# Optimization experiments

Hardware: AMD Instinct MI355X
Metric: run time of the kernel (lower is better)

The kernel has to match this reference:

```python
import jax, jax.numpy as jnp
import numpy as np


def _shift_kernel(dtype=jnp.float32):
    # IdealDelayKernels: 9 output channels, 8 one-hot 3x3 shift taps (center skipped), 9th all-zero
    k = np.zeros((9, 1, 1, 3, 3), np.float32)
    idx = -1
    for i in range(3):
        for j in range(3):
            if i == 1 and j == 1:
                continue
            idx += 1
            k[idx, 0, 0, i, j] = 1.0
    return jnp.asarray(k, dtype)


def _conv2d(x, w, b, pad):
    y = jax.lax.conv_general_dilated(x, w, (1, 1), [(pad, pad), (pad, pad)],
                                     dimension_numbers=('NCHW', 'OIHW', 'NCHW'))
    return y if b is None else y + b[None, :, None, None]


def setup_inputs() -> dict:
    key = jax.random.key(0)
    ks = jax.random.split(key, 16)
    B, C, H, W = 2, 19, 512, 512
    s = 0.1  # xavier-ish scale for small convs
    return {
        'x': jax.random.normal(ks[0], (B, C, H, W), jnp.float32),
        'image': jax.random.normal(ks[1], (B, 3, H, W), jnp.float32),
        # IntraNetwork(3 -> 16 -> 16 -> 19): conv3x3, conv3x3, conv1x1 (BN frozen at identity)
        'intra_w1': jax.random.normal(ks[2], (16, 3, 3, 3), jnp.float32) * s,
        'intra_b1': jnp.zeros((16,), jnp.float32),
        'intra_w2': jax.random.normal(ks[3], (16, 16, 3, 3), jnp.float32) * s,
        'intra_b2': jnp.zeros((16,), jnp.float32),
        'intra_w3': jax.random.normal(ks[4], (19, 16, 1, 1), jnp.float32) * s,
        'intra_b3': jnp.zeros((19,), jnp.float32),
        # GuidingNetwork(20 -> 32 -> 32 -> 11): conv3x3, conv3x3, conv1x1 + sigmoid
        'guide_w1': jax.random.normal(ks[5], (32, 20, 3, 3), jnp.float32) * s,
        'guide_b1': jnp.zeros((32,), jnp.float32),
        'guide_w2': jax.random.normal(ks[6], (32, 32, 3, 3), jnp.float32) * s,
        'guide_b2': jnp.zeros((32,), jnp.float32),
        'guide_w3': jax.random.normal(ks[7], (11, 32, 1, 1), jnp.float32) * s,
        'guide_b3': jnp.zeros((11,), jnp.float32),
    }


def reference(x, image, intra_w1, intra_b1, intra_w2, intra_b2, intra_w3, intra_b3,
              guide_w1, guide_b1, guide_w2, guide_b2, guide_w3, guide_b3):
    # intra_net: image -> [B,19,H,W] (frozen BN == identity)
    f = jax.nn.relu(_conv2d(image, intra_w1, intra_b1, 1))
    f = jax.nn.relu(_conv2d(f, intra_w2, intra_b2, 1))
    intra = _conv2d(f, intra_w3, intra_b3, 0)            # [B,19,H,W]

    # Laplacian edge on the argmax label map
    single_x = jnp.argmax(x, axis=1, keepdims=True).astype(x.dtype)  # [B,1,H,W]
    lapla = jnp.full((1, 1, 3, 3), 1.0, x.dtype).at[0, 0, 1, 1].set(-8.0)
    edge = _conv2d(single_x, lapla, None, 1)             # [B,1,H,W]

    # guiding network: cat(intra, edge) -> 11 per-pixel guide weights
    gi = jnp.concatenate([intra, edge], axis=1)          # [B,20,H,W]
    g = jax.nn.relu(_conv2d(gi, guide_w1, guide_b1, 1))
    g = jax.nn.relu(_conv2d(g, guide_w2, guide_b2, 1))
    g = jax.nn.sigmoid(_conv2d(g, guide_w3, guide_b3, 0))  # [B,11,H,W]
    guide_feat = g[:, :, None]                           # [B,11,1,H,W]
    guide_feat = guide_feat / (jnp.sum(guide_feat, axis=1, keepdims=True) + 1e-9)

    # shift-kernel conv3d: [B,1,19,H,W] -> [B,9,19,H,W]
    xs = x[:, None]
    short = jax.lax.conv_general_dilated(xs, _shift_kernel(x.dtype), (1, 1, 1),
                                         [(0, 0), (1, 1), (1, 1)],
                                         dimension_numbers=('NCDHW', 'OIDHW', 'NCDHW'))
    xcat = jnp.concatenate([xs, short, intra[:, None]], axis=1)  # [B,11,19,H,W]

    out = jnp.sum(guide_feat * xcat, axis=1)             # [B,19,H,W]
    return (out, guide_feat, edge)
```

## Files before the change

kernel.cpp:

```cpp
#include <hip/hip_runtime.h>
#include <math.h>

constexpr int H = 512, W = 512, B = 2;
constexpr int HW = H * W;

typedef __attribute__((ext_vector_type(8))) short short8;
typedef __attribute__((ext_vector_type(4))) float floatx4;
typedef __attribute__((ext_vector_type(4))) unsigned int uint4v;

__device__ inline unsigned short f2bf(float f) {
  union { float f; unsigned int u; } x{f};
  const unsigned int u = x.u;
  return (unsigned short)((u + 0x7FFFu + ((u >> 16) & 1u)) >> 16);
}
__device__ inline float bf2f(unsigned short s) {
  union { unsigned int u; float f; } x;
  x.u = (unsigned int)s << 16;
  return x.f;
}
__device__ inline void unpk2(unsigned int u, float& lo, float& hi) {
  union { unsigned int u; float f; } a, b;
  a.u = u << 16;
  b.u = u & 0xffff0000u;
  lo = a.f;
  hi = b.f;
}

template <int CIN, int COUT, bool RELU>
__global__ __launch_bounds__(256) void conv3x3_fp32_pack(
    const float* __restrict__ in0, const float* __restrict__ wgt,
    const float* __restrict__ bias, unsigned short* __restrict__ outp) {
  constexpr int TS = 16, TH = 18, LDW = 20;
  __shared__ float tile[CIN][TH][LDW];
  const int tx = threadIdx.x, ty = threadIdx.y;
  const int tid = ty * 16 + tx;
  const int w0 = blockIdx.x * TS, h0 = blockIdx.y * TS, b = blockIdx.z;

  for (int idx = tid; idx < CIN * TH * TH; idx += 256) {
    const int cin = idx / (TH * TH);
    const int rem = idx - cin * (TH * TH);
    const int r = rem / TH, c = rem - r * TH;
    const int gh = h0 + r - 1, gw = w0 + c - 1;
    float v = 0.f;
    if ((unsigned)gh < (unsigned)H && (unsigned)gw < (unsigned)W)
      v = in0[(size_t)(b * CIN + cin) * HW + gh * W + gw];
    tile[cin][r][c] = v;
  }
  __syncthreads();

  float acc[COUT];
#pragma unroll
  for (int co = 0; co < COUT; ++co) acc[co] = bias[co];
  for (int cin = 0; cin < CIN; ++cin) {
#pragma unroll
    for (int t = 0; t < 9; ++t) {
      const int ky = t / 3, kx = t - ky * 3;
      const float v = tile[cin][ty + ky][tx + kx];
#pragma unroll
      for (int co = 0; co < COUT; ++co)
        acc[co] = fmaf(v, wgt[(co * CIN + cin) * 9 + t], acc[co]);
    }
  }
  const int oh = h0 + ty, ow = w0 + tx;
  unsigned int pk[COUT / 2];
#pragma unroll
  for (int c2 = 0; c2 < COUT / 2; ++c2) {
    float a0 = acc[2 * c2], a1 = acc[2 * c2 + 1];
    if (RELU) { a0 = fmaxf(a0, 0.f); a1 = fmaxf(a1, 0.f); }
    pk[c2] = (unsigned)f2bf(a0) | ((unsigned)f2bf(a1) << 16);
  }
  unsigned short* dst = outp + ((size_t)(b * H + oh) * W + ow) * COUT;
#pragma unroll
  for (int u = 0; u < COUT / 8; ++u)
    *(uint4v*)(dst + u * 8) = uint4v{pk[u * 4], pk[u * 4 + 1], pk[u * 4 + 2], pk[u * 4 + 3]};
}

template <int CIN, int CINP, int COUT, int KS>
__global__ __launch_bounds__(256) void repack_w(
    const float* __restrict__ w, unsigned short* __restrict__ bp) {
  constexpr int NT = COUT / 16;
  const int idx = blockIdx.x * 256 + threadIdx.x;
  if (idx >= NT * KS * 512) return;
  const int j = idx & 7;
  const int l = (idx >> 3) & 63;
  const int ks = (idx >> 9) % KS;
  const int nt = idx / (KS * 512);
  const int co = nt * 16 + (l & 15);
  const int kglob = ks * 32 + (l >> 4) * 8 + j;
  const int tap = kglob / CINP;
  const int cin = kglob % CINP;
  float v = 0.f;
  if (tap < 9 && cin < CIN) v = w[((size_t)co * CIN + cin) * 9 + tap];
  bp[idx] = f2bf(v);
}

template <int CINP, int KS, int NT, bool EDGE19, int EPI>
__global__ __launch_bounds__(256) void conv3x3_mfma(
    const unsigned short* __restrict__ inp, const float* __restrict__ edg,
    const unsigned short* __restrict__ bpack, const float* __restrict__ bias,
    const float* __restrict__ ew, const float* __restrict__ eb,
    unsigned short* __restrict__ outp, float* __restrict__ outf) {
  constexpr int COUT = NT * 16;
  constexpr int CS = (CINP == 16) ? 24 : 40;
  constexpr int EPS = (EPI == 1) ? 24 : 40;
  constexpr int TR = 10;
  __shared__ __align__(16) unsigned short tile[TR * 34 * CS];

  const int tid = threadIdx.x;
  const int w0 = blockIdx.x * 32, h0 = blockIdx.y * 8, b = blockIdx.z;

  for (int idx = tid; idx < TR * 34; idx += 256) {
    const int r = idx / 34, c = idx - r * 34;
    const int gh = h0 + r - 1, gw = w0 + c - 1;
    unsigned short* dst = tile + (size_t)(r * 34 + c) * CS;
    if ((unsigned)gh < (unsigned)H && (unsigned)gw < (unsigned)W) {
      const unsigned short* src = inp + ((size_t)(b * H + gh) * W + gw) * CINP;
#pragma unroll
      for (int u = 0; u < CINP / 8; ++u)
        *(uint4v*)(dst + u * 8) = *(const uint4v*)(src + u * 8);
      if (EDGE19) dst[19] = f2bf(edg[(size_t)b * HW + gh * W + gw]);
    } else {
#pragma unroll
      for (int u = 0; u < CINP / 8; ++u)
        *(uint4v*)(dst + u * 8) = uint4v{0, 0, 0, 0};
    }
  }
  __syncthreads();

  const int wv = tid >> 6, lane = tid & 63;
  const int q = lane >> 4, l15 = lane & 15;
  const int rb = wv * 2;

  floatx4 acc[4][NT];
#pragma unroll
  for (int mf = 0; mf < 4; ++mf)
#pragma unroll
    for (int nt = 0; nt < NT; ++nt) acc[mf][nt] = floatx4{0.f, 0.f, 0.f, 0.f};

#pragma unroll
  for (int ks = 0; ks < KS; ++ks) {
    short8 bfrag[NT];
#pragma unroll
    for (int nt = 0; nt < NT; ++nt)
      bfrag[nt] = *(const short8*)(bpack + (size_t)(((nt * KS) + ks) * 64 + lane) * 8);

    const int kbase = ks * 32;
    const int kq = kbase + q * 8;
    int tapq = kq / CINP;
    const int cinq = kq % CINP;
    if (tapq > 8) tapq = 8;
    const int ky = tapq / 3, kx = tapq - ky * 3;
    const unsigned short* aptr =
        tile + (size_t)((rb + ky) * 34 + (l15 + kx)) * CS + cinq;

#pragma unroll
    for (int mf = 0; mf < 4; ++mf) {
      constexpr int mfs[4][2] = {{0, 0}, {0, 16}, {1, 0}, {1, 16}};
      const int off = (mfs[mf][0] * 34 + mfs[mf][1]) * CS;
      const short8 af = *(const short8*)(aptr + off);
#pragma unroll
      for (int nt = 0; nt < NT; ++nt)
        acc[mf][nt] = __builtin_amdgcn_mfma_f32_16x16x32_bf16(
            af, bfrag[nt], acc[mf][nt], 0, 0, 0);
    }
  }

  if constexpr (EPI == 0) {
#pragma unroll
    for (int nt = 0; nt < NT; ++nt) {
      const float bv = bias[nt * 16 + l15];
#pragma unroll
      for (int mf = 0; mf < 4; ++mf) {
        const int row = mf >> 1, colb = (mf & 1) * 16 + q * 4;
        unsigned short* dst =
            outp + ((size_t)(b * H + h0 + rb + row) * W + w0) * COUT + nt * 16 + l15;
#pragma unroll
        for (int rg = 0; rg < 4; ++rg) {
          const float v = fmaxf(acc[mf][nt][rg] + bv, 0.f);
          dst[(size_t)(colb + rg) * COUT] = f2bf(v);
        }
      }
    }
  } else {
    __syncthreads();
#pragma unroll
    for (int nt = 0; nt < NT; ++nt) {
      const float bv = bias[nt * 16 + l15];
#pragma unroll
      for (int mf = 0; mf < 4; ++mf) {
        const int row = rb + (mf >> 1), colb = (mf & 1) * 16 + q * 4;
#pragma unroll
        for (int rg = 0; rg < 4; ++rg) {
          const int px = row * 32 + colb + rg;
          tile[(size_t)px * EPS + nt * 16 + l15] =
              f2bf(fmaxf(acc[mf][nt][rg] + bv, 0.f));
        }
      }
    }
    __syncthreads();

    {
      const int p = tid;
      const int gh = h0 + (p >> 5), gw = w0 + (p & 31);
      const unsigned short* src = tile + (size_t)p * EPS;

      if constexpr (EPI == 1) {
        float xi[16];
        const uint4v r0 = *(const uint4v*)src;
        const uint4v r1 = *(const uint4v*)(src + 8);
        unpk2(r0.x, xi[0], xi[1]);   unpk2(r0.y, xi[2], xi[3]);
        unpk2(r0.z, xi[4], xi[5]);   unpk2(r0.w, xi[6], xi[7]);
        unpk2(r1.x, xi[8], xi[9]);   unpk2(r1.y, xi[10], xi[11]);
        unpk2(r1.z, xi[12], xi[13]); unpk2(r1.w, xi[14], xi[15]);
        float a[19];
#pragma unroll
        for (int co = 0; co < 19; ++co) a[co] = eb[co];
#pragma unroll
        for (int c = 0; c < 16; ++c) {
          const float v = xi[c];
#pragma unroll
          for (int co = 0; co < 19; ++co) a[co] = fmaf(v, ew[co * 16 + c], a[co]);
        }
        unsigned int pk[12];
#pragma unroll
        for (int j = 0; j < 9; ++j)
          pk[j] = (unsigned)f2bf(a[2 * j]) | ((unsigned)f2bf(a[2 * j + 1]) << 16);
        pk[9] = (unsigned)f2bf(a[18]);
        pk[10] = 0; pk[11] = 0;
        unsigned short* dst = outp + ((size_t)(b * H + gh) * W + gw) * 24;
#pragma unroll
        for (int u = 0; u < 3; ++u)
          *(uint4v*)(dst + u * 8) =
              uint4v{pk[u * 4], pk[u * 4 + 1], pk[u * 4 + 2], pk[u * 4 + 3]};
      } else {
        float xi[32];
#pragma unroll
        for (int u = 0; u < 4; ++u) {
          const uint4v r = *(const uint4v*)(src + u * 8);
          unpk2(r.x, xi[u * 8 + 0], xi[u * 8 + 1]);
          unpk2(r.y, xi[u * 8 + 2], xi[u * 8 + 3]);
          unpk2(r.z, xi[u * 8 + 4], xi[u * 8 + 5]);
          unpk2(r.w, xi[u * 8 + 6], xi[u * 8 + 7]);
        }
        float g[11], sum = 0.f;
#pragma unroll
        for (int co = 0; co < 11; ++co) {
          float a = eb[co];
#pragma unroll
          for (int c = 0; c < 32; ++c) a = fmaf(xi[c], ew[co * 32 + c], a);
          g[co] = 1.f / (1.f + expf(-a));
          sum += g[co];
        }
        const float inv = 1.f / (sum + 1e-9f);
        const size_t s = (size_t)gh * W + gw;
#pragma unroll
        for (int co = 0; co < 11; ++co)
          outf[(size_t)(b * 11 + co) * HW + s] = g[co] * inv;
      }
    }
  }
}

__global__ __launch_bounds__(256) void argmax_kernel(
    const float* __restrict__ x, float* __restrict__ sx) {
  const int t = blockIdx.x * 256 + threadIdx.x;
  const int b = t >> 18;
  const int s = t & (HW - 1);
  const float* xp = x + (size_t)b * 19 * HW + s;
  float bv = *xp;
  float ix = 0.f;
#pragma unroll
  for (int c = 1; c < 19; ++c) {
    const float v = xp[(size_t)c * HW];
    if (v > bv) { bv = v; ix = (float)c; }
  }
  sx[(size_t)b * HW + s] = ix;
}

__device__ inline void load_row4(const float* __restrict__ plane, int hh,
                                 int w0, float r[4]) {
#pragma unroll
  for (int i = 0; i < 4; ++i) r[i] = 0.f;
  if ((unsigned)hh < (unsigned)H) {
    const float* rp = plane + (size_t)hh * W + w0;
    const float2 m = *(const float2*)rp;
    r[1] = m.x; r[2] = m.y;
    if (w0 > 0) r[0] = rp[-1];
    if (w0 + 2 < W) r[3] = rp[2];
  }
}

__global__ __launch_bounds__(256) void edge_kernel(
    const float* __restrict__ sx, float* __restrict__ edge) {
  const int t = blockIdx.x * 256 + threadIdx.x;
  const int b = t / (HW / 2);
  const int s2 = (t - b * (HW / 2)) * 2;
  const int h = s2 / W, w0 = s2 - h * W;
  const float* sp = sx + (size_t)b * HW;
  float r0[4], r1[4], r2[4];
  load_row4(sp, h - 1, w0, r0);
  load_row4(sp, h, w0, r1);
  load_row4(sp, h + 1, w0, r2);
  float o[2];
#pragma unroll
  for (int k = 0; k < 2; ++k)
    o[k] = r0[k] + r0[k + 1] + r0[k + 2] + r1[k] + r1[k + 2] + r2[k] +
           r2[k + 1] + r2[k + 2] - 8.f * r1[k + 1];
  *(float2*)(edge + (size_t)b * HW + s2) = float2{o[0], o[1]};
}

__device__ inline void load_row3(const float* __restrict__ plane, int hh,
                                 int w, float r[3]) {
  r[0] = 0.f; r[1] = 0.f; r[2] = 0.f;
  if ((unsigned)hh < (unsigned)H) {
    const float* rp = plane + (size_t)hh * W + w;
    r[1] = rp[0];
    if (w > 0) r[0] = rp[-1];
    if (w + 1 < W) r[2] = rp[1];
  }
}

__global__ __launch_bounds__(256) void combine_kernel(
    const float* __restrict__ x, const unsigned short* __restrict__ intp,
    const float* __restrict__ gf, float* __restrict__ out) {
  const int t = blockIdx.x * 256 + threadIdx.x;
  const int b = t >> 18;
  const int s = t & (HW - 1);
  const int h = s >> 9, w = s & (W - 1);
  const float* gp = gf + (size_t)b * 11 * HW + s;

  float g[11];
#pragma unroll
  for (int m = 0; m < 11; ++m) {
    if (m == 9) continue;
    g[m] = gp[(size_t)m * HW];
  }

  const unsigned short* ip = intp + ((size_t)b * HW + s) * 24;
  for (int c = 0; c < 19; ++c) {
    const float* xc = x + (size_t)(b * 19 + c) * HW;
    float r0[3], r1[3], r2[3];
    load_row3(xc, h - 1, w, r0);
    load_row3(xc, h, w, r1);
    load_row3(xc, h + 1, w, r2);
    const float itv = bf2f(ip[c]);
    float a = g[0] * r1[1];
    a = fmaf(g[1], r0[0], a);
    a = fmaf(g[2], r0[1], a);
    a = fmaf(g[3], r0[2], a);
    a = fmaf(g[4], r1[0], a);
    a = fmaf(g[5], r1[2], a);
    a = fmaf(g[6], r2[0], a);
    a = fmaf(g[7], r2[1], a);
    a = fmaf(g[8], r2[2], a);
    a = fmaf(g[10], itv, a);
    out[(size_t)(b * 19 + c) * HW + s] = a;
  }
}

extern "C" void kernel_launch(void* const* d_in, const int* in_sizes, int n_in,
                              void* d_out, int out_size, void* d_ws,
                              size_t ws_size, hipStream_t stream) {
  const float* x     = (const float*)d_in[0];
  const float* image = (const float*)d_in[1];
  const float* iw1 = (const float*)d_in[2];
  const float* ib1 = (const float*)d_in[3];
  const float* iw2 = (const float*)d_in[4];
  const float* ib2 = (const float*)d_in[5];
  const float* iw3 = (const float*)d_in[6];
  const float* ib3 = (const float*)d_in[7];
  const float* gw1 = (const float*)d_in[8];
  const float* gb1 = (const float*)d_in[9];
  const float* gw2 = (const float*)d_in[10];
  const float* gb2 = (const float*)d_in[11];
  const float* gw3 = (const float*)d_in[12];
  const float* gb3 = (const float*)d_in[13];

  float* ws = (float*)d_ws;
  float* sx = ws;
  unsigned short* f1p  = (unsigned short*)(ws + (size_t)2 * HW);
  unsigned short* intp = (unsigned short*)(ws + (size_t)34 * HW);
  unsigned short* g1p  = (unsigned short*)(ws + (size_t)58 * HW);
  unsigned short* bp_ic2 = (unsigned short*)(ws + (size_t)122 * HW);
  unsigned short* bp_gc1 = bp_ic2 + 4096;
  unsigned short* bp_gc2 = bp_gc1 + 12288;

  float* out0 = (float*)d_out;
  float* gfo  = out0 + (size_t)2 * 19 * HW;
  float* edg  = gfo + (size_t)2 * 11 * HW;

  const dim3 blk16(16, 16);
  const dim3 grd16(W / 16, H / 16, B);
  const dim3 grdM(W / 32, H / 8, B);
  const int flat1 = (B * HW) / 256;
  const int flat2 = (B * HW / 2) / 256;

  argmax_kernel<<<flat1, 256, 0, stream>>>(x, sx);
  edge_kernel<<<flat2, 256, 0, stream>>>(sx, edg);

  repack_w<16, 16, 16, 5><<<10, 256, 0, stream>>>(iw2, bp_ic2);
  repack_w<20, 24, 32, 7><<<28, 256, 0, stream>>>(gw1, bp_gc1);
  repack_w<32, 32, 32, 9><<<36, 256, 0, stream>>>(gw2, bp_gc2);

  conv3x3_fp32_pack<3, 16, true><<<grd16, blk16, 0, stream>>>(image, iw1, ib1, f1p);
  conv3x3_mfma<16, 5, 1, false, 1><<<grdM, 256, 0, stream>>>(
      f1p, nullptr, bp_ic2, ib2, iw3, ib3, intp, nullptr);
  conv3x3_mfma<24, 7, 2, true, 0><<<grdM, 256, 0, stream>>>(
      intp, edg, bp_gc1, gb1, nullptr, nullptr, g1p, nullptr);
  conv3x3_mfma<32, 9, 2, false, 2><<<grdM, 256, 0, stream>>>(
      g1p, nullptr, bp_gc2, gb2, gw3, gb3, nullptr, gfo);

  combine_kernel<<<flat1, 256, 0, stream>>>(x, intp, gfo, out0);
}
```

Baseline: 242.7 us.

## Fuse guided combine into the final guiding-conv epilogue

```diff
diff --git a/kernel.cpp b/kernel.cpp
--- a/kernel.cpp
+++ b/kernel.cpp
@@ -24,6 +24,17 @@
   b.u = u & 0xffff0000u;
   lo = a.f;
   hi = b.f;
+}
+
+__device__ inline void load_row3(const float* __restrict__ plane, int hh,
+                                 int w, float r[3]) {
+  r[0] = 0.f; r[1] = 0.f; r[2] = 0.f;
+  if ((unsigned)hh < (unsigned)H) {
+    const float* rp = plane + (size_t)hh * W + w;
+    r[1] = rp[0];
+    if (w > 0) r[0] = rp[-1];
+    if (w + 1 < W) r[2] = rp[1];
+  }
 }
 
 template <int CIN, int COUT, bool RELU>
@@ -99,7 +110,9 @@
     const unsigned short* __restrict__ inp, const float* __restrict__ edg,
     const unsigned short* __restrict__ bpack, const float* __restrict__ bias,
     const float* __restrict__ ew, const float* __restrict__ eb,
-    unsigned short* __restrict__ outp, float* __restrict__ outf) {
+    unsigned short* __restrict__ outp, float* __restrict__ outf,
+    const float* __restrict__ xin, const unsigned short* __restrict__ ipn,
+    float* __restrict__ outc) {
   constexpr int COUT = NT * 16;
   constexpr int CS = (CINP == 16) ? 24 : 40;
   constexpr int EPS = (EPI == 1) ? 24 : 40;
@@ -256,6 +269,32 @@
 #pragma unroll
         for (int co = 0; co < 11; ++co)
           outf[(size_t)(b * 11 + co) * HW + s] = g[co] * inv;
+
+        if constexpr (EPI == 3) {
+          float gn[11];
+#pragma unroll
+          for (int m = 0; m < 11; ++m) gn[m] = g[m] * inv;
+          const unsigned short* ip = ipn + ((size_t)b * HW + s) * 24;
+          for (int c = 0; c < 19; ++c) {
+            const float* xc = xin + (size_t)(b * 19 + c) * HW;
+            float r0[3], r1[3], r2[3];
+            load_row3(xc, gh - 1, gw, r0);
+            load_row3(xc, gh, gw, r1);
+            load_row3(xc, gh + 1, gw, r2);
+            const float itv = bf2f(ip[c]);
+            float a = gn[0] * r1[1];
+            a = fmaf(gn[1], r0[0], a);
+            a = fmaf(gn[2], r0[1], a);
+            a = fmaf(gn[3], r0[2], a);
+            a = fmaf(gn[4], r1[0], a);
+            a = fmaf(gn[5], r1[2], a);
+            a = fmaf(gn[6], r2[0], a);
+            a = fmaf(gn[7], r2[1], a);
+            a = fmaf(gn[8], r2[2], a);
+            a = fmaf(gn[10], itv, a);
+            outc[(size_t)(b * 19 + c) * HW + s] = a;
+          }
+        }
       }
     }
   }
@@ -307,55 +346,6 @@
     o[k] = r0[k] + r0[k + 1] + r0[k + 2] + r1[k] + r1[k + 2] + r2[k] +
            r2[k + 1] + r2[k + 2] - 8.f * r1[k + 1];
   *(float2*)(edge + (size_t)b * HW + s2) = float2{o[0], o[1]};
-}
-
-__device__ inline void load_row3(const float* __restrict__ plane, int hh,
-                                 int w, float r[3]) {
-  r[0] = 0.f; r[1] = 0.f; r[2] = 0.f;
-  if ((unsigned)hh < (unsigned)H) {
-    const float* rp = plane + (size_t)hh * W + w;
-    r[1] = rp[0];
-    if (w > 0) r[0] = rp[-1];
-    if (w + 1 < W) r[2] = rp[1];
-  }
-}
-
-__global__ __launch_bounds__(256) void combine_kernel(
-    const float* __restrict__ x, const unsigned short* __restrict__ intp,
-    const float* __restrict__ gf, float* __restrict__ out) {
-  const int t = blockIdx.x * 256 + threadIdx.x;
-  const int b = t >> 18;
-  const int s = t & (HW - 1);
-  const int h = s >> 9, w = s & (W - 1);
-  const float* gp = gf + (size_t)b * 11 * HW + s;
-
-  float g[11];
-#pragma unroll
-  for (int m = 0; m < 11; ++m) {
-    if (m == 9) continue;
-    g[m] = gp[(size_t)m * HW];
-  }
-
-  const unsigned short* ip = intp + ((size_t)b * HW + s) * 24;
-  for (int c = 0; c < 19; ++c) {
-    const float* xc = x + (size_t)(b * 19 + c) * HW;
-    float r0[3], r1[3], r2[3];
-    load_row3(xc, h - 1, w, r0);
-    load_row3(xc, h, w, r1);
-    load_row3(xc, h + 1, w, r2);
-    const float itv = bf2f(ip[c]);
-    float a = g[0] * r1[1];
-    a = fmaf(g[1], r0[0], a);
-    a = fmaf(g[2], r0[1], a);
-    a = fmaf(g[3], r0[2], a);
-    a = fmaf(g[4], r1[0], a);
-    a = fmaf(g[5], r1[2], a);
-    a = fmaf(g[6], r2[0], a);
-    a = fmaf(g[7], r2[1], a);
-    a = fmaf(g[8], r2[2], a);
-    a = fmaf(g[10], itv, a);
-    out[(size_t)(b * 19 + c) * HW + s] = a;
-  }
 }
 
 extern "C" void kernel_launch(void* const* d_in, const int* in_sizes, int n_in,
@@ -404,11 +394,9 @@
 
   conv3x3_fp32_pack<3, 16, true><<<grd16, blk16, 0, stream>>>(image, iw1, ib1, f1p);
   conv3x3_mfma<16, 5, 1, false, 1><<<grdM, 256, 0, stream>>>(
-      f1p, nullptr, bp_ic2, ib2, iw3, ib3, intp, nullptr);
+      f1p, nullptr, bp_ic2, ib2, iw3, ib3, intp, nullptr, nullptr, nullptr, nullptr);
   conv3x3_mfma<24, 7, 2, true, 0><<<grdM, 256, 0, stream>>>(
-      intp, edg, bp_gc1, gb1, nullptr, nullptr, g1p, nullptr);
-  conv3x3_mfma<32, 9, 2, false, 2><<<grdM, 256, 0, stream>>>(
-      g1p, nullptr, bp_gc2, gb2, gw3, gb3, nullptr, gfo);
-
-  combine_kernel<<<flat1, 256, 0, stream>>>(x, intp, gfo, out0);
-}
+      intp, edg, bp_gc1, gb1, nullptr, nullptr, g1p, nullptr, nullptr, nullptr, nullptr);
+  conv3x3_mfma<32, 9, 2, false, 3><<<grdM, 256, 0, stream>>>(
+      g1p, nullptr, bp_gc2, gb2, gw3, gb3, nullptr, gfo, x, intp, out0);
+}
```

New measurement: 237.8 us. 1.02x faster.
